# Kernel optimization log

Hardware: AMD Instinct MI355X
Metric: run time of the kernel (lower is better)

The kernel has to match this reference:

```python
import jax, jax.numpy as jnp
import numpy as np


def setup_inputs() -> dict:
    key = jax.random.key(0)
    ks = jax.random.split(key, 4)
    B, C, H, W = 4, 512, 64, 64
    A = 512  # attention_dim
    x = jax.random.normal(ks[0], (B, C, H, W), dtype=jnp.float32)
    # 1x1 conv weights as [out_ch, in_ch] matrices (kaiming-like scale)
    scale = np.sqrt(2.0 / C).astype(np.float32)
    Wq = jax.random.normal(ks[1], (A, C), dtype=jnp.float32) * scale
    Wk = jax.random.normal(ks[2], (A, C), dtype=jnp.float32) * scale
    Wv = jax.random.normal(ks[3], (C, C), dtype=jnp.float32) * scale
    bq = jnp.zeros((A,), dtype=jnp.float32)
    bk = jnp.zeros((A,), dtype=jnp.float32)
    bv = jnp.zeros((C,), dtype=jnp.float32)
    return {"x": x, "Wq": Wq, "bq": bq, "Wk": Wk, "bk": bk, "Wv": Wv, "bv": bv}


def reference(x, Wq, bq, Wk, bk, Wv, bv):
    B, C, H, W = x.shape
    N = H * W
    xf = x.reshape(B, C, N)  # [B, C, N]
    # 1x1 convs == per-pixel channel matmuls
    q = jnp.einsum('ac,bcn->bna', Wq, xf) + bq[None, None, :]   # [B, N, A] (query, permuted)
    k = jnp.einsum('ac,bcn->ban', Wk, xf) + bk[None, :, None]   # [B, A, N] (key)
    v = jnp.einsum('oc,bcn->bno', Wv, xf) + bv[None, None, :]   # [B, N, C] (value, permuted)
    attn = jnp.einsum('bna,bam->bnm', q, k)                     # [B, N, N]
    attn = jax.nn.softmax(attn, axis=-2)                        # softmax over dim=-2 (queries)
    out = jnp.einsum('bnm,bmc->bnc', attn, v)                   # [B, N, C]
    # Faithful to torch: .view(B, C, H, W) reinterprets the [B, N, C] buffer
    out = out.reshape(B, C, H, W)
    return x + 0.1 * out
```

## Files before the change

kernel.cpp:

```cpp
#include <hip/hip_runtime.h>
#include <stdint.h>


typedef _Float16 f16x8 __attribute__((ext_vector_type(8)));
typedef float f32x4 __attribute__((ext_vector_type(4)));

__device__ __forceinline__ void dma16(const void* g, void* l) {
  __builtin_amdgcn_global_load_lds(
      (const __attribute__((address_space(1))) uint32_t*)(uintptr_t)g,
      (__attribute__((address_space(3))) uint32_t*)(uint32_t)(uintptr_t)l, 16, 0, 0);
}

__device__ __forceinline__ uint16_t f2bf(float f) {
  uint32_t u = __float_as_uint(f);
  u += 0x7FFFu + ((u >> 16) & 1u);
  return (uint16_t)(u >> 16);
}

template <int ASRC, int EPI>
__global__ void __launch_bounds__(256, 2) gemm_f16(
    const _Float16* __restrict__ Ap, long lda, long zsa,
    const _Float16* __restrict__ Bp, long ldb, long zsb,
    int kslice,
    const _Float16* __restrict__ fs16, long zsl,
    float* __restrict__ outF, _Float16* __restrict__ outH, long ldc, long zso,
    const float* __restrict__ bias0, const float* __restrict__ bias1,
    const float* __restrict__ xadd,
    float* __restrict__ pmax, float* __restrict__ psum, long zsp,
    float alpha)
{
  __shared__ _Float16 smem[8192];
  _Float16* sA = smem;
  _Float16* sB = smem + 4096;

  const int z = blockIdx.z;
  const long i0 = (long)blockIdx.x * 128;
  const long j0 = (long)blockIdx.y * 128;
  const int t = (int)threadIdx.x;
  const int lane = t & 63;
  const int wv = t >> 6;
  const int quad = lane >> 4;
  const int lrow = lane & 15;
  const int wm = (wv & 1) << 6;
  const int wn = (wv >> 1) << 6;

  const int idx0 = wv * 2;
  const int srow = lane >> 2;
  const int sseg = (lane & 3) << 3;
  const _Float16* gA0 = Ap + z * zsa + (i0 + idx0 * 16 + srow) * lda + sseg;
  const _Float16* gA1 = gA0 + 16 * lda;
  const _Float16* gB0 = Bp + z * zsb + (j0 + idx0 * 16 + srow) * ldb + sseg;
  const _Float16* gB1 = gB0 + 16 * ldb;
  _Float16* lA0 = sA + idx0 * 512;
  _Float16* lA1 = lA0 + 512;
  _Float16* lB0 = sB + idx0 * 512;
  _Float16* lB1 = lB0 + 512;

  const _Float16* fsZ = nullptr;
  if constexpr (ASRC == 1)
    fsZ = fs16 + z * zsl + (long)blockIdx.x * 4096 + quad * 8;

  f32x4 acc[4][4];
  const f32x4 fz = {0.f, 0.f, 0.f, 0.f};
#pragma unroll
  for (int a = 0; a < 4; a++)
#pragma unroll
    for (int b = 0; b < 4; b++) acc[a][b] = fz;

  for (int kk = 0; kk < kslice; kk += 32) {
    __syncthreads();
    dma16(gA0 + kk, lA0);
    dma16(gA1 + kk, lA1);
    dma16(gB0 + kk, lB0);
    dma16(gB1 + kk, lB1);
    __syncthreads();

    f16x8 fa[4], fb[4];
#pragma unroll
    for (int f = 0; f < 4; f++) {
      fa[f] = *(const f16x8*)&sA[(wm + f * 16 + lrow) * 32 + quad * 8];
      fb[f] = *(const f16x8*)&sB[(wn + f * 16 + lrow) * 32 + quad * 8];
    }
    if constexpr (ASRC == 1) {
      const f16x8 fsv = *(const f16x8*)(fsZ + kk);
#pragma unroll
      for (int f = 0; f < 4; f++) fa[f] = fa[f] * fsv;
    }
#pragma unroll
    for (int fm = 0; fm < 4; fm++)
#pragma unroll
      for (int fn = 0; fn < 4; fn++)
        acc[fm][fn] = __builtin_amdgcn_mfma_f32_16x16x32_f16(fa[fm], fb[fn], acc[fm][fn], 0, 0, 0);
  }

  const long obase = (long)z * zso;

  if constexpr (EPI == 1 || EPI == 2) {
#pragma unroll
    for (int fm = 0; fm < 4; fm++) {
      const long gi0 = i0 + wm + fm * 16 + quad * 4;
#pragma unroll
      for (int fn = 0; fn < 4; fn++) {
        const long gj = j0 + wn + fn * 16 + lrow;
        float badd = 0.f;
        if constexpr (EPI == 1) badd = (gj < 512) ? bias0[gj] : bias1[gj - 512];
#pragma unroll
        for (int r = 0; r < 4; r++) {
          float v = acc[fm][fn][r];
          if constexpr (EPI == 1) v += badd;
          else v += bias0[gi0 + r];
          outH[obase + (gi0 + r) * ldc + gj] = (_Float16)v;
        }
      }
    }
  } else if constexpr (EPI == 3) {
#pragma unroll
    for (int fm = 0; fm < 4; fm++) {
      const long gi0 = i0 + wm + fm * 16 + quad * 4;
#pragma unroll
      for (int fn = 0; fn < 4; fn++) {
        const long gj = j0 + wn + fn * 16 + lrow;
#pragma unroll
        for (int r = 0; r < 4; r++) {
          const long o = obase + (gi0 + r) * ldc + gj;
          outF[o] = fmaf(alpha, acc[fm][fn][r], xadd[o]);
        }
      }
    }
  } else {
    __syncthreads();
    float* Ls = (float*)smem;
#pragma unroll
    for (int fn = 0; fn < 4; fn++) {
      float mx = -3.4e38f;
#pragma unroll
      for (int fm = 0; fm < 4; fm++)
#pragma unroll
        for (int r = 0; r < 4; r++) mx = fmaxf(mx, acc[fm][fn][r]);
      float sm = 0.f;
#pragma unroll
      for (int fm = 0; fm < 4; fm++)
#pragma unroll
        for (int r = 0; r < 4; r++) sm += __expf(acc[fm][fn][r] - mx);
      Ls[(wv * 4 + quad) * 64 + fn * 16 + lrow] = mx;
      Ls[1024 + (wv * 4 + quad) * 64 + fn * 16 + lrow] = sm;
    }
    __syncthreads();
    {
      const int c = t & 127;
      const int h = t >> 7;
      const int wvv = ((c >> 6) << 1) + h;
      const int wc = c & 63;
      float M = -3.4e38f, Ss = 0.f;
#pragma unroll
      for (int q = 0; q < 4; q++) {
        float m2 = Ls[(wvv * 4 + q) * 64 + wc];
        float s2 = Ls[1024 + (wvv * 4 + q) * 64 + wc];
        float nm = fmaxf(M, m2);
        Ss = Ss * __expf(M - nm) + s2 * __expf(m2 - nm);
        M = nm;
      }
      Ls[2048 + h * 128 + c] = M;
      Ls[2304 + h * 128 + c] = Ss;
    }
    __syncthreads();
    if (t < 128) {
      float m0 = Ls[2048 + t], m1 = Ls[2048 + 128 + t];
      float sa = Ls[2304 + t], sb = Ls[2304 + 128 + t];
      float nm = fmaxf(m0, m1);
      float s = sa * __expf(m0 - nm) + sb * __expf(m1 - nm);
      const long pidx = z * zsp + (long)blockIdx.x * 4096 + j0 + t;
      pmax[pidx] = nm;
      psum[pidx] = s;
      Ls[t] = nm;
    }
    __syncthreads();
#pragma unroll
    for (int fn = 0; fn < 4; fn++) {
      const int colc = wn + fn * 16 + lrow;
      const float Mcol = Ls[colc];
      const long gj = j0 + colc;
#pragma unroll
      for (int fm = 0; fm < 4; fm++) {
        const long gi0 = i0 + wm + fm * 16 + quad * 4;
#pragma unroll
        for (int r = 0; r < 4; r++)
          outH[obase + (gi0 + r) * ldc + gj] = (_Float16)__expf(acc[fm][fn][r] - Mcol);
      }
    }
  }
}

__global__ void convert_weights(const float* __restrict__ Wq, const float* __restrict__ Wk,
                                const float* __restrict__ Wv,
                                _Float16* __restrict__ WQK, _Float16* __restrict__ Wv16)
{
  int idx = blockIdx.x * 256 + threadIdx.x;
  if (idx < 524288)
    WQK[idx] = (_Float16)((idx < 262144) ? Wq[idx] : Wk[idx - 262144]);
  else
    Wv16[idx - 524288] = (_Float16)Wv[idx - 524288];
}

__global__ void transpose_x(const float* __restrict__ x, _Float16* __restrict__ xT)
{
  __shared__ float tile[32][33];
  const int b = blockIdx.z;
  const int n0 = blockIdx.x * 32;
  const int c0 = blockIdx.y * 32;
  const int tx = threadIdx.x;
  const int ty = threadIdx.y;
  const float* xb = x + (long)b * 2097152;
#pragma unroll
  for (int k = 0; k < 4; k++)
    tile[ty + k * 8][tx] = xb[(long)(c0 + ty + k * 8) * 4096 + n0 + tx];
  __syncthreads();
  _Float16* xTb = xT + (long)b * 2097152;
#pragma unroll
  for (int k = 0; k < 4; k++)
    xTb[(long)(n0 + ty + k * 8) * 512 + c0 + tx] = (_Float16)tile[tx][ty + k * 8];
}

__global__ void stats_final(const float* __restrict__ pmax, const float* __restrict__ psum,
                            float* __restrict__ lse)
{
  const int idx = blockIdx.x * 256 + threadIdx.x;
  const int z = idx >> 12;
  const int m = idx & 4095;
  const float* pm = pmax + (long)z * 131072 + m;
  const float* ps = psum + (long)z * 131072 + m;
  float M = -3.4e38f, S = 0.f;
  for (int i = 0; i < 32; i++) {
    float m2 = pm[(long)i * 4096], s2 = ps[(long)i * 4096];
    float nm = fmaxf(M, m2);
    S = S * __expf(M - nm) + s2 * __expf(m2 - nm);
    M = nm;
  }
  lse[idx] = M + __logf(S);
}

__global__ void scale_factors(const float* __restrict__ pmax, const float* __restrict__ lse,
                              _Float16* __restrict__ fs16)
{
  const int idx = blockIdx.x * 256 + threadIdx.x;
  const int z = idx >> 17;
  const int m = idx & 4095;
  fs16[idx] = (_Float16)__expf(pmax[idx] - lse[(z << 12) + m]);
}

extern "C" void kernel_launch(void* const* d_in, const int* in_sizes, int n_in,
                              void* d_out, int out_size, void* d_ws, size_t ws_size,
                              hipStream_t stream)
{
  const float* x  = (const float*)d_in[0];
  const float* Wq = (const float*)d_in[1];
  const float* bq = (const float*)d_in[2];
  const float* Wk = (const float*)d_in[3];
  const float* bk = (const float*)d_in[4];
  const float* Wv = (const float*)d_in[5];
  const float* bv = (const float*)d_in[6];
  float* out = (float*)d_out;

  char* w = (char*)d_ws;
  _Float16* WQK   = (_Float16*)(w + 0);
  _Float16* Wv16  = (_Float16*)(w + 1048576);
  _Float16* xT    = (_Float16*)(w + 1572864);
  _Float16* QK    = (_Float16*)(w + 18350080);
  _Float16* Vt    = (_Float16*)(w + 51904512);
  float*    lse   = (float*)   (w + 68681728);
  float*    pmaxB = (float*)   (w + 68747264);
  float*    psumB = (float*)   (w + 70844416);
  _Float16* fs16  = (_Float16*)(w + 72941568);
  _Float16* S16   = (_Float16*)(w + 75038720);

  convert_weights<<<3072, 256, 0, stream>>>(Wq, Wk, Wv, WQK, Wv16);
  transpose_x<<<dim3(128, 16, 4), dim3(32, 8), 0, stream>>>(x, xT);

  gemm_f16<0, 1><<<dim3(32, 8, 4), 256, 0, stream>>>(
      xT, 512, 2097152L, WQK, 512, 0L, 512, nullptr, 0L,
      nullptr, QK, 1024, 4194304L, bq, bk, nullptr, nullptr, nullptr, 0L, 0.f);
  gemm_f16<0, 2><<<dim3(4, 32, 4), 256, 0, stream>>>(
      Wv16, 512, 0L, xT, 512, 2097152L, 512, nullptr, 0L,
      nullptr, Vt, 4096, 2097152L, bv, nullptr, nullptr, nullptr, nullptr, 0L, 0.f);
  gemm_f16<0, 4><<<dim3(32, 32, 4), 256, 0, stream>>>(
      QK, 1024, 4194304L, QK + 512, 1024, 4194304L, 512, nullptr, 0L,
      nullptr, S16, 4096, 16777216L, nullptr, nullptr, nullptr,
      pmaxB, psumB, 131072L, 0.f);
  stats_final<<<64, 256, 0, stream>>>(pmaxB, psumB, lse);
  scale_factors<<<2048, 256, 0, stream>>>(pmaxB, lse, fs16);
  gemm_f16<1, 3><<<dim3(32, 4, 4), 256, 0, stream>>>(
      S16, 4096, 16777216L, Vt, 4096, 2097152L, 4096, fs16, 131072L,
      out, nullptr, 512, 2097152L, nullptr, nullptr, x, nullptr, nullptr, 0L, 0.1f);
}
```

Baseline: 381.4 us.

## Stage GEMM tiles through registers with padded LDS and K=64 steps

Replaces the direct global-to-LDS DMA loads with register-staged vector loads written into LDS rows padded to 40 halves, and processes two 32-wide K sub-tiles per barrier pair. The padding is meant to remove LDS bank conflicts on the fragment reads, and the larger K step halves the number of synchronizations. The fs scale multiply now happens once on the loaded tile instead of on every warp's fragments. In exchange it uses more LDS and registers per block, which may lower occupancy, and loses the asynchronous DMA path.

```diff
diff --git a/kernel.cpp b/kernel.cpp
--- a/kernel.cpp
+++ b/kernel.cpp
@@ -2,20 +2,11 @@
 #include <stdint.h>
 
 
+#define LDT 40
+#define SUB 5120
+
 typedef _Float16 f16x8 __attribute__((ext_vector_type(8)));
 typedef float f32x4 __attribute__((ext_vector_type(4)));
-
-__device__ __forceinline__ void dma16(const void* g, void* l) {
-  __builtin_amdgcn_global_load_lds(
-      (const __attribute__((address_space(1))) uint32_t*)(uintptr_t)g,
-      (__attribute__((address_space(3))) uint32_t*)(uint32_t)(uintptr_t)l, 16, 0, 0);
-}
-
-__device__ __forceinline__ uint16_t f2bf(float f) {
-  uint32_t u = __float_as_uint(f);
-  u += 0x7FFFu + ((u >> 16) & 1u);
-  return (uint16_t)(u >> 16);
-}
 
 template <int ASRC, int EPI>
 __global__ void __launch_bounds__(256, 2) gemm_f16(
@@ -29,9 +20,11 @@
     float* __restrict__ pmax, float* __restrict__ psum, long zsp,
     float alpha)
 {
-  __shared__ _Float16 smem[8192];
-  _Float16* sA = smem;
-  _Float16* sB = smem + 4096;
+  __shared__ _Float16 smem[4 * SUB];
+  _Float16* sA0 = smem;
+  _Float16* sA1 = smem + SUB;
+  _Float16* sB0 = smem + 2 * SUB;
+  _Float16* sB1 = smem + 3 * SUB;
 
   const int z = blockIdx.z;
   const long i0 = (long)blockIdx.x * 128;
@@ -44,21 +37,19 @@
   const int wm = (wv & 1) << 6;
   const int wn = (wv >> 1) << 6;
 
-  const int idx0 = wv * 2;
-  const int srow = lane >> 2;
-  const int sseg = (lane & 3) << 3;
-  const _Float16* gA0 = Ap + z * zsa + (i0 + idx0 * 16 + srow) * lda + sseg;
-  const _Float16* gA1 = gA0 + 16 * lda;
-  const _Float16* gB0 = Bp + z * zsb + (j0 + idx0 * 16 + srow) * ldb + sseg;
-  const _Float16* gB1 = gB0 + 16 * ldb;
-  _Float16* lA0 = sA + idx0 * 512;
-  _Float16* lA1 = lA0 + 512;
-  _Float16* lB0 = sB + idx0 * 512;
-  _Float16* lB1 = lB0 + 512;
+  const int r0 = t >> 2;
+  const int s0 = (t & 3) << 3;
+
+  const _Float16* gA0 = Ap + z * zsa + (i0 + r0) * lda + s0;
+  const _Float16* gA1 = gA0 + 64 * lda;
+  const _Float16* gB0 = Bp + z * zsb + (j0 + r0) * ldb + s0;
+  const _Float16* gB1 = gB0 + 64 * ldb;
+  const int la0 = r0 * LDT + s0;
+  const int la1 = (r0 + 64) * LDT + s0;
 
   const _Float16* fsZ = nullptr;
   if constexpr (ASRC == 1)
-    fsZ = fs16 + z * zsl + (long)blockIdx.x * 4096 + quad * 8;
+    fsZ = fs16 + z * zsl + (long)blockIdx.x * 4096 + s0;
 
   f32x4 acc[4][4];
   const f32x4 fz = {0.f, 0.f, 0.f, 0.f};
@@ -67,30 +58,50 @@
 #pragma unroll
     for (int b = 0; b < 4; b++) acc[a][b] = fz;
 
-  for (int kk = 0; kk < kslice; kk += 32) {
-    __syncthreads();
-    dma16(gA0 + kk, lA0);
-    dma16(gA1 + kk, lA1);
-    dma16(gB0 + kk, lB0);
-    dma16(gB1 + kk, lB1);
-    __syncthreads();
-
-    f16x8 fa[4], fb[4];
-#pragma unroll
-    for (int f = 0; f < 4; f++) {
-      fa[f] = *(const f16x8*)&sA[(wm + f * 16 + lrow) * 32 + quad * 8];
-      fb[f] = *(const f16x8*)&sB[(wn + f * 16 + lrow) * 32 + quad * 8];
-    }
+  for (int kk = 0; kk < kslice; kk += 64) {
+    f16x8 va0 = *(const f16x8*)(gA0 + kk);
+    f16x8 va1 = *(const f16x8*)(gA1 + kk);
+    f16x8 va2 = *(const f16x8*)(gA0 + kk + 32);
+    f16x8 va3 = *(const f16x8*)(gA1 + kk + 32);
+    f16x8 vb0 = *(const f16x8*)(gB0 + kk);
+    f16x8 vb1 = *(const f16x8*)(gB1 + kk);
+    f16x8 vb2 = *(const f16x8*)(gB0 + kk + 32);
+    f16x8 vb3 = *(const f16x8*)(gB1 + kk + 32);
     if constexpr (ASRC == 1) {
-      const f16x8 fsv = *(const f16x8*)(fsZ + kk);
-#pragma unroll
-      for (int f = 0; f < 4; f++) fa[f] = fa[f] * fsv;
-    }
-#pragma unroll
-    for (int fm = 0; fm < 4; fm++)
-#pragma unroll
-      for (int fn = 0; fn < 4; fn++)
-        acc[fm][fn] = __builtin_amdgcn_mfma_f32_16x16x32_f16(fa[fm], fb[fn], acc[fm][fn], 0, 0, 0);
+      const f16x8 fsv0 = *(const f16x8*)(fsZ + kk);
+      const f16x8 fsv1 = *(const f16x8*)(fsZ + kk + 32);
+      va0 = va0 * fsv0;
+      va1 = va1 * fsv0;
+      va2 = va2 * fsv1;
+      va3 = va3 * fsv1;
+    }
+    __syncthreads();
+    *(f16x8*)&sA0[la0] = va0;
+    *(f16x8*)&sA0[la1] = va1;
+    *(f16x8*)&sA1[la0] = va2;
+    *(f16x8*)&sA1[la1] = va3;
+    *(f16x8*)&sB0[la0] = vb0;
+    *(f16x8*)&sB0[la1] = vb1;
+    *(f16x8*)&sB1[la0] = vb2;
+    *(f16x8*)&sB1[la1] = vb3;
+    __syncthreads();
+
+#pragma unroll
+    for (int h = 0; h < 2; h++) {
+      const _Float16* pA = h ? sA1 : sA0;
+      const _Float16* pB = h ? sB1 : sB0;
+      f16x8 fa[4], fb[4];
+#pragma unroll
+      for (int f = 0; f < 4; f++) {
+        fa[f] = *(const f16x8*)&pA[(wm + f * 16 + lrow) * LDT + quad * 8];
+        fb[f] = *(const f16x8*)&pB[(wn + f * 16 + lrow) * LDT + quad * 8];
+      }
+#pragma unroll
+      for (int fm = 0; fm < 4; fm++)
+#pragma unroll
+        for (int fn = 0; fn < 4; fn++)
+          acc[fm][fn] = __builtin_amdgcn_mfma_f32_16x16x32_f16(fa[fm], fb[fn], acc[fm][fn], 0, 0, 0);
+    }
   }
 
   const long obase = (long)z * zso;
```

New measurement: 314.0 us. -17.7%, faster.
